# Kernel tuning notes

Measured on AMD Instinct MI355X. Metric: run time of the kernel, lower is better.

The kernel has to match this reference:

```python
import jax, jax.numpy as jnp
import numpy as np

N, E, C, NB, NE, G = 20000, 320000, 64, 8, 4, 16
L2 = 9          # (max_ell+1)^2 with max_ell=2
RMAX = 5.0
HID = 16        # nonlinear readout hidden width


def setup_inputs():
    key = jax.random.key(0)
    ks = jax.random.split(key, 16)
    positions = jax.random.uniform(ks[0], (N, 3), dtype=jnp.float32) * 3.0
    elems = jax.random.randint(ks[1], (N,), 0, NE)
    node_attrs = jax.nn.one_hot(elems, NE, dtype=jnp.float32)
    edge_index = jax.random.randint(ks[2], (2, E), 0, N)
    batch = jnp.sort(jax.random.randint(ks[3], (N,), 0, G))
    shifts = jnp.zeros((E, 3), jnp.float32)
    atomic_energies = jnp.array([-1.0, -2.0, -3.0, -4.0], jnp.float32)
    sc = lambda k, shp, fan: jax.random.normal(k, shp, jnp.float32) / np.sqrt(fan).astype(np.float32)
    W_embed = sc(ks[4], (NE, C), NE)
    W_up = sc(ks[5], (2, C, C), C)
    W1 = sc(ks[6], (2, NB, 64), NB)
    W2 = sc(ks[7], (2, 64, C), 64)
    W_out = sc(ks[8], (2, C, C), C)
    W_skip = sc(ks[9], (2, NE, C), NE)
    w_read0 = sc(ks[10], (C,), C)
    W_r1 = sc(ks[11], (C, HID), C)
    w_r2 = sc(ks[12], (HID,), HID)
    return dict(positions=positions, node_attrs=node_attrs, shifts=shifts,
                atomic_energies=atomic_energies, W_embed=W_embed, W_up=W_up,
                W1=W1, W2=W2, W_out=W_out, W_skip=W_skip, w_read0=w_read0,
                W_r1=W_r1, w_r2=w_r2, edge_index=edge_index, batch=batch)


def _sph_harm_l2(u):
    # component-normalized real spherical harmonics up to l=2 on unit vectors
    x, y, z = u[:, 0], u[:, 1], u[:, 2]
    s3, s5, s15 = jnp.sqrt(3.0), jnp.sqrt(5.0), jnp.sqrt(15.0)
    return jnp.stack([jnp.ones_like(x),
                      s3 * x, s3 * y, s3 * z,
                      s15 * x * y, s15 * y * z, 0.5 * s5 * (3.0 * z * z - 1.0),
                      s15 * x * z, 0.5 * s15 * (x * x - y * y)], axis=-1)


def _radial(r):
    # Bessel radial basis with polynomial cutoff (p=6)
    n = jnp.arange(1, NB + 1, dtype=jnp.float32)
    rb = jnp.sqrt(2.0 / RMAX) * jnp.sin(n * jnp.pi * r[:, None] / RMAX) / r[:, None]
    u = r / RMAX
    fc = 1.0 - 28.0 * u**6 + 48.0 * u**7 - 21.0 * u**8
    fc = jnp.where(u < 1.0, fc, 0.0)
    return rb * fc[:, None]


def _energy_contributions(positions, node_attrs, shifts, atomic_energies,
                          W_embed, W_up, W1, W2, W_out, W_skip,
                          w_read0, W_r1, w_r2, edge_index, batch):
    snd, rcv = edge_index[0], edge_index[1]
    vec = positions[snd] - positions[rcv] + shifts                  # [E,3]
    r = jnp.sqrt(jnp.sum(vec * vec, axis=-1) + 1e-12)               # [E]
    Y = _sph_harm_l2(vec / r[:, None])                              # [E,L2]
    ef = _radial(r)                                                 # [E,NB]
    # E0: per-element reference energies, summed per graph
    e0 = jax.ops.segment_sum(node_attrs @ atomic_energies, batch, num_segments=G)
    h0 = node_attrs @ W_embed                                       # [N,C] scalar feats
    h = jnp.zeros((positions.shape[0], L2, C), h0.dtype).at[:, 0, :].set(h0)
    readouts = [lambda s: s @ w_read0,
                lambda s: jax.nn.silu(s @ W_r1) @ w_r2]             # linear / nonlinear
    energies = [e0]
    for i in range(2):
        hu = jnp.einsum('nlc,cd->nld', h, W_up[i])                  # channel mix
        R = jax.nn.silu(ef @ W1[i]) @ W2[i]                         # radial MLP [E,C]
        s = jnp.einsum('elc,el->ec', hu[snd], Y)                    # equivariant contraction
        m = Y[:, :, None] * (R * s)[:, None, :]                     # [E,L2,C] messages
        agg = jax.ops.segment_sum(m, rcv, num_segments=positions.shape[0])
        h = jnp.einsum('nlc,cd->nld', agg, W_out[i])
        h = h.at[:, 0, :].add(node_attrs @ W_skip[i])               # scalar skip connection
        node_en = readouts[i](h[:, 0, :])                           # [N]
        energies.append(jax.ops.segment_sum(node_en, batch, num_segments=G))
    return jnp.stack(energies, axis=-1)                             # [G, num_interactions+1]


def reference(positions, node_attrs, shifts, atomic_energies, W_embed, W_up,
              W1, W2, W_out, W_skip, w_read0, W_r1, w_r2, edge_index, batch):
    contributions = _energy_contributions(positions, node_attrs, shifts,
        atomic_energies, W_embed, W_up, W1, W2, W_out, W_skip,
        w_read0, W_r1, w_r2, edge_index, batch)
    total_energy = jnp.sum(contributions, axis=-1)                  # [G]
    forces = -jax.grad(lambda p: jnp.sum(_energy_contributions(p, node_attrs,
        shifts, atomic_energies, W_embed, W_up, W1, W2, W_out, W_skip,
        w_read0, W_r1, w_r2, edge_index, batch)))(positions)        # [N,3]
    return total_energy, contributions, forces
```

## Files before the change

kernel.cpp:

```cpp
#include <hip/hip_runtime.h>
#include <cmath>

constexpr int N_  = 20000;
constexpr int E_  = 320000;
constexpr int NE_ = 4;
constexpr int G_  = 16;
constexpr int CAP = 96;
constexpr float RMAXF = 5.0f;
constexpr float PI_F  = 3.14159265358979323846f;
constexpr float S3  = 1.7320508075688772f;
constexpr float S5  = 2.2360679774997896f;
constexpr float S15 = 3.8729833462074170f;
constexpr float KC_ = 0.6324555320336759f;

typedef unsigned short u16;
typedef unsigned int   u32;
typedef _Float16 f16;
typedef _Float16 f16x2 __attribute__((ext_vector_type(2)));

#define DEV static __device__ __forceinline__

__device__ float g_fallback[110000000];

DEV float sigmoidf_(float x){ return 1.0f/(1.0f+__expf(-x)); }

DEV float b2f(u16 u){ return __uint_as_float(((u32)u)<<16); }
DEV u16  f2b(float f){
  u32 x = __float_as_uint(f);
  return (u16)((x + 0x7FFFu + ((x>>16)&1u)) >> 16);
}
DEV u16  f2h(float f){ union{f16 h; u16 u;} v; v.h=(f16)f; return v.u; }
DEV float h2f(u16 u){ union{u16 u2; f16 h;} v; v.u2=u; return (float)v.h; }

DEV f16x2 u2h(u32 x){ union{u32 u; f16x2 h;} v; v.u=x; return v.h; }
DEV u32 h2u(f16x2 h){ union{u32 u; f16x2 h;} v; v.h=h; return v.u; }
DEV u32 pkh(float a, float b){ f16x2 h; h.x=(f16)a; h.y=(f16)b; return h2u(h); }

DEV void st8(float* p, const float* d){
  ((float4*)p)[0] = make_float4(d[0],d[1],d[2],d[3]);
  ((float4*)p)[1] = make_float4(d[4],d[5],d[6],d[7]);
}
DEV void ld4(const float* __restrict__ p, float* d){
  float4 a = ((const float4*)p)[0];
  d[0]=a.x; d[1]=a.y; d[2]=a.z; d[3]=a.w;
}
DEV void ld4b(const u16* __restrict__ p, float* d){
  ushort4 a = *(const ushort4*)p;
  d[0]=b2f(a.x); d[1]=b2f(a.y); d[2]=b2f(a.z); d[3]=b2f(a.w);
}
DEV void ld4h(const u16* __restrict__ p, float* d){
  ushort4 a = *(const ushort4*)p;
  d[0]=h2f(a.x); d[1]=h2f(a.y); d[2]=h2f(a.z); d[3]=h2f(a.w);
}
DEV void st8b(u16* p, const float* d){
  uint4 v;
  v.x = (u32)f2b(d[0]) | ((u32)f2b(d[1])<<16);
  v.y = (u32)f2b(d[2]) | ((u32)f2b(d[3])<<16);
  v.z = (u32)f2b(d[4]) | ((u32)f2b(d[5])<<16);
  v.w = (u32)f2b(d[6]) | ((u32)f2b(d[7])<<16);
  *(uint4*)p = v;
}
DEV void st8h(u16* p, const float* d){
  uint4 v;
  v.x = pkh(d[0],d[1]); v.y = pkh(d[2],d[3]);
  v.z = pkh(d[4],d[5]); v.w = pkh(d[6],d[7]);
  *(uint4*)p = v;
}

__global__ void k_csr(const int* __restrict__ ei, int* __restrict__ cntR, int* __restrict__ cntS,
                      int* __restrict__ listR, int* __restrict__ listS){
  int e = blockIdx.x*256 + threadIdx.x;
  int s = ei[e], r = ei[E_+e];
  int p = atomicAdd(&cntR[r], 1); if (p < CAP) listR[r*CAP+p] = e;
  int q = atomicAdd(&cntS[s], 1); if (q < CAP) listS[s*CAP+q] = e;
}

__global__ void k_pre(const float* __restrict__ Wout0, const float* __restrict__ Wup1,
                      const float* __restrict__ Wskip0, const float* __restrict__ wread0,
                      float* __restrict__ WA, float* __restrict__ sa,
                      float* __restrict__ va, float* __restrict__ sv){
  int t = threadIdx.x;
  for (int idx=t; idx<4096; idx+=256){
    int c = idx>>6, d = idx&63;
    float acc=0.f;
    for (int m=0;m<64;++m) acc += Wout0[c*64+m]*Wup1[m*64+d];
    WA[idx]=acc;
  }
  {
    int k = t>>6, d = t&63;
    float acc=0.f;
    for (int m=0;m<64;++m) acc += Wskip0[k*64+m]*Wup1[m*64+d];
    sa[t]=acc;
  }
  if (t<64){
    float acc=0.f;
    for (int d=0;d<64;++d) acc += Wout0[t*64+d]*wread0[d];
    va[t]=acc;
  }
  if (t<4){
    float acc=0.f;
    for (int d=0;d<64;++d) acc += Wskip0[t*64+d]*wread0[d];
    sv[t]=acc;
  }
}

__global__ __launch_bounds__(256, 2)
void k_fwd_edge(const float* __restrict__ pos, const float* __restrict__ shifts,
                const int* __restrict__ ei,
                const float* __restrict__ W1g, const float* __restrict__ W2g,
                float* __restrict__ Y, float* __restrict__ u3,
                float* __restrict__ irr,
                u16* __restrict__ R0, u16* __restrict__ R1,
                u16* __restrict__ q0, u16* __restrict__ q1){
  __shared__ float sW1[1024];
  __shared__ u32   sW2h[4096];
  __shared__ u32   sAh[32*36];
  int t = threadIdx.x;
  for (int i=t;i<1024;i+=256) sW1[i]=W1g[i];
  for (int i=t;i<4096;i+=256){
    int L = i>>11, rem = i&2047, kp = rem>>6, c = rem&63;
    sW2h[i] = pkh(W2g[L*4096 + (2*kp)*64 + c], W2g[L*4096 + (2*kp+1)*64 + c]);
  }
  __syncthreads();
  int wid=t>>6, lane=t&63, q=lane>>3, j=lane&7, c0=j*8;
  int slot = wid*8 + q;
  int e = blockIdx.x*32 + slot;
  int snd = ei[e], rcv = ei[E_+e];
  float vx = pos[snd*3+0]-pos[rcv*3+0]+shifts[(size_t)e*3+0];
  float vy = pos[snd*3+1]-pos[rcv*3+1]+shifts[(size_t)e*3+1];
  float vz = pos[snd*3+2]-pos[rcv*3+2]+shifts[(size_t)e*3+2];
  float ss = vx*vx+vy*vy+vz*vz + 1e-12f;
  float rad = sqrtf(ss);
  float inv = 1.0f/rad;
  float x = vx*inv, y = vy*inv, z = vz*inv;
  float tt = rad*(1.0f/RMAXF);
  float fc = 0.0f, dfc = 0.0f;
  if (tt < 1.0f){
    float t2=tt*tt, t4=t2*t2, t5=t4*tt, t6=t5*tt, t7=t6*tt, t8=t7*tt;
    fc  = 1.0f - 28.0f*t6 + 48.0f*t7 - 21.0f*t8;
    dfc = (-168.0f*t5 + 336.0f*t6 - 168.0f*t7)*(1.0f/RMAXF);
  }
  float th = rad*(PI_F/RMAXF);
  float s1 = __sinf(th), c1 = __cosf(th);
  float base = KC_*inv*fc;
  float efv[8], gfv[8];
  {
    float sb = s1, cb = c1;
    #pragma unroll
    for (int b=0;b<8;++b){
      efv[b] = base*sb;
      float wb_ = (float)(b+1)*(PI_F/RMAXF);
      float rb  = KC_*sb*inv;
      float drb = KC_*(wb_*cb - sb*inv)*inv;
      gfv[b] = drb*fc + rb*dfc;
      float sn = sb*c1 + cb*s1;
      cb = cb*c1 - sb*s1;
      sb = sn;
    }
  }
  if (j==0){
    irr[e]=inv;
    u3[(size_t)e*3+0]=x; u3[(size_t)e*3+1]=y; u3[(size_t)e*3+2]=z;
    float* Ye = Y + (size_t)e*9;
    Ye[0]=1.0f;
    Ye[1]=S3*x; Ye[2]=S3*y; Ye[3]=S3*z;
    Ye[4]=S15*x*y; Ye[5]=S15*y*z;
    Ye[6]=0.5f*S5*(3.0f*z*z-1.0f);
    Ye[7]=S15*x*z;
    Ye[8]=0.5f*S15*(x*x-y*y);
  }
  u32* myAh = sAh + slot*36;
  for (int L=0; L<2; ++L){
    const float* w1 = sW1 + L*512;
    const u32*  w2h = sW2h + L*2048;
    float zz[8]={0,0,0,0,0,0,0,0};
    float wgv[8]={0,0,0,0,0,0,0,0};
    #pragma unroll 4
    for (int b=0;b<8;++b){
      float efb = efv[b], gfb = gfv[b];
      const float4* w=(const float4*)(w1 + b*64 + c0);
      float4 wa=w[0], wb=w[1];
      zz[0]+=efb*wa.x; zz[1]+=efb*wa.y; zz[2]+=efb*wa.z; zz[3]+=efb*wa.w;
      zz[4]+=efb*wb.x; zz[5]+=efb*wb.y; zz[6]+=efb*wb.z; zz[7]+=efb*wb.w;
      wgv[0]+=gfb*wa.x; wgv[1]+=gfb*wa.y; wgv[2]+=gfb*wa.z; wgv[3]+=gfb*wa.w;
      wgv[4]+=gfb*wb.x; wgv[5]+=gfb*wb.y; wgv[6]+=gfb*wb.z; wgv[7]+=gfb*wb.w;
    }
    float a[8], dv[8];
    #pragma unroll
    for (int i=0;i<8;++i){
      float sg = sigmoidf_(zz[i]);
      a[i]  = zz[i]*sg;
      float sp = sg*(1.0f + zz[i]*(1.0f - sg));
      dv[i] = wgv[i]*sp;
    }
    {
      uint4 av;
      av.x = pkh(a[0],a[1]); av.y = pkh(a[2],a[3]);
      av.z = pkh(a[4],a[5]); av.w = pkh(a[6],a[7]);
      *(uint4*)(myAh + 4*j) = av;
    }
    {
      float r0=0.f,r1=0.f,r2=0.f,r3=0.f,r4=0.f,r5=0.f,r6=0.f,r7=0.f;
      #pragma unroll 2
      for (int kp4=0; kp4<8; ++kp4){
        uint4 dq = *(const uint4*)(myAh + 4*kp4);
        #pragma unroll
        for (int i=0;i<4;++i){
          u32 du = (i==0)?dq.x:(i==1)?dq.y:(i==2)?dq.z:dq.w;
          f16x2 dh = u2h(du);
          const u32* wrow = w2h + (4*kp4+i)*64 + c0;
          uint4 w0 = *(const uint4*)(wrow);
          uint4 w1v = *(const uint4*)(wrow+4);
          r0 = __builtin_amdgcn_fdot2(dh, u2h(w0.x),  r0, false);
          r1 = __builtin_amdgcn_fdot2(dh, u2h(w0.y),  r1, false);
          r2 = __builtin_amdgcn_fdot2(dh, u2h(w0.z),  r2, false);
          r3 = __builtin_amdgcn_fdot2(dh, u2h(w0.w),  r3, false);
          r4 = __builtin_amdgcn_fdot2(dh, u2h(w1v.x), r4, false);
          r5 = __builtin_amdgcn_fdot2(dh, u2h(w1v.y), r5, false);
          r6 = __builtin_amdgcn_fdot2(dh, u2h(w1v.z), r6, false);
          r7 = __builtin_amdgcn_fdot2(dh, u2h(w1v.w), r7, false);
        }
      }
      float racc[8] = {r0,r1,r2,r3,r4,r5,r6,r7};
      st8b((L ? R1 : R0) + (size_t)e*64 + c0, racc);
    }
    {
      uint4 av;
      av.x = pkh(dv[0],dv[1]); av.y = pkh(dv[2],dv[3]);
      av.z = pkh(dv[4],dv[5]); av.w = pkh(dv[6],dv[7]);
      *(uint4*)(myAh + 4*j) = av;
    }
    {
      float r0=0.f,r1=0.f,r2=0.f,r3=0.f,r4=0.f,r5=0.f,r6=0.f,r7=0.f;
      #pragma unroll 2
      for (int kp4=0; kp4<8; ++kp4){
        uint4 dq = *(const uint4*)(myAh + 4*kp4);
        #pragma unroll
        for (int i=0;i<4;++i){
          u32 du = (i==0)?dq.x:(i==1)?dq.y:(i==2)?dq.z:dq.w;
          f16x2 dh = u2h(du);
          const u32* wrow = w2h + (4*kp4+i)*64 + c0;
          uint4 w0 = *(const uint4*)(wrow);
          uint4 w1v = *(const uint4*)(wrow+4);
          r0 = __builtin_amdgcn_fdot2(dh, u2h(w0.x),  r0, false);
          r1 = __builtin_amdgcn_fdot2(dh, u2h(w0.y),  r1, false);
          r2 = __builtin_amdgcn_fdot2(dh, u2h(w0.z),  r2, false);
          r3 = __builtin_amdgcn_fdot2(dh, u2h(w0.w),  r3, false);
          r4 = __builtin_amdgcn_fdot2(dh, u2h(w1v.x), r4, false);
          r5 = __builtin_amdgcn_fdot2(dh, u2h(w1v.y), r5, false);
          r6 = __builtin_amdgcn_fdot2(dh, u2h(w1v.z), r6, false);
          r7 = __builtin_amdgcn_fdot2(dh, u2h(w1v.w), r7, false);
        }
      }
      float qacc[8] = {r0,r1,r2,r3,r4,r5,r6,r7};
      st8h((L ? q1 : q0) + (size_t)e*64 + c0, qacc);
    }
  }
}

__global__ void k_e0(const float* __restrict__ attrs, const float* __restrict__ ae,
                     const int* __restrict__ batch, float* __restrict__ out){
  __shared__ float bins[G_];
  int t = threadIdx.x;
  if (t < G_) bins[t] = 0.f;
  __syncthreads();
  int n = blockIdx.x*256 + t;
  if (n < N_){
    float v = 0.f;
    #pragma unroll
    for (int k=0;k<NE_;++k) v += attrs[n*NE_+k]*ae[k];
    atomicAdd(&bins[batch[n]], v);
  }
  __syncthreads();
  if (t < G_){
    float b = bins[t];
    if (b != 0.f){
      atomicAdd(&out[t], b);
      atomicAdd(&out[G_ + t*3 + 0], b);
    }
  }
}

__global__ void k_wembup(const float* __restrict__ Wemb, const float* __restrict__ Wup0,
                         float* __restrict__ WembUp){
  int t = threadIdx.x; int k = t>>6, c = t&63;
  float acc = 0.f;
  for (int j=0;j<64;++j) acc += Wemb[k*64+j]*Wup0[j*64+c];
  WembUp[k*64+c] = acc;
}

__global__ void k_hu0(const float* __restrict__ attrs, const float* __restrict__ WembUp,
                      float* __restrict__ hu0){
  int i = blockIdx.x*256 + threadIdx.x;
  int n = i>>6, c = i&63;
  float acc = 0.f;
  #pragma unroll
  for (int k=0;k<NE_;++k) acc += attrs[n*NE_+k]*WembUp[k*64+c];
  hu0[i] = acc;
}

__global__ void k_agg0(const int* __restrict__ cntR, const int* __restrict__ listR,
                       const int* __restrict__ ei, const float* __restrict__ hu0,
                       const u16* __restrict__ R0, const float* __restrict__ Y,
                       float* __restrict__ agg0){
  int t = threadIdx.x; int n = blockIdx.x*4 + (t>>6); int c = t&63;
  float acc[9] = {0,0,0,0,0,0,0,0,0};
  int deg = min(cntR[n], CAP);
  #pragma unroll 2
  for (int j=0;j<deg;++j){
    int e = listR[n*CAP+j];
    int s = ei[e];
    float p = b2f(R0[(size_t)e*64+c])*hu0[(size_t)s*64+c];
    #pragma unroll
    for (int l=0;l<9;++l) acc[l] += Y[(size_t)e*9+l]*p;
  }
  #pragma unroll
  for (int l=0;l<9;++l) agg0[((size_t)n*9+l)*64+c] = acc[l];
}

__global__ void k_s1(const int* __restrict__ cntS, const int* __restrict__ listS,
                     const u16* __restrict__ hu1, const float* __restrict__ Y,
                     u16* __restrict__ s1){
  int t = threadIdx.x; int n = blockIdx.x*4 + (t>>6); int c = t&63;
  float hu[9];
  #pragma unroll
  for (int l=0;l<9;++l) hu[l] = b2f(hu1[((size_t)n*9+l)*64+c]);
  int deg = min(cntS[n], CAP);
  #pragma unroll 2
  for (int j=0;j<deg;++j){
    int e = listS[n*CAP+j];
    float acc = 0.f;
    #pragma unroll
    for (int l=0;l<9;++l) acc += hu[l]*Y[(size_t)e*9+l];
    s1[(size_t)e*64+c] = f2h(acc);
  }
}

__global__ void k_agg1(const int* __restrict__ cntR, const int* __restrict__ listR,
                       const u16* __restrict__ R1, const u16* __restrict__ s1,
                       float* __restrict__ agg1){
  int t = threadIdx.x; int n = blockIdx.x*4 + (t>>6); int c = t&63;
  float acc = 0.f;
  int deg = min(cntR[n], CAP);
  #pragma unroll 2
  for (int j=0;j<deg;++j){
    int e = listR[n*CAP+j];
    acc += b2f(R1[(size_t)e*64+c])*h2f(s1[(size_t)e*64+c]);
  }
  agg1[(size_t)n*64+c] = acc;
}

__global__ void k_dhu1(const int* __restrict__ cntS, const int* __restrict__ listS,
                       const int* __restrict__ ei, const u16* __restrict__ R1,
                       const float* __restrict__ ga1, const float* __restrict__ Y,
                       float* __restrict__ dhu1){
  int t = threadIdx.x; int n = blockIdx.x*4 + (t>>6); int c = t&63;
  float acc[9] = {0,0,0,0,0,0,0,0,0};
  int deg = min(cntS[n], CAP);
  #pragma unroll 2
  for (int j=0;j<deg;++j){
    int e = listS[n*CAP+j];
    int r = ei[E_+e];
    float ds = b2f(R1[(size_t)e*64+c])*ga1[(size_t)r*64+c];
    #pragma unroll
    for (int l=0;l<9;++l) acc[l] += Y[(size_t)e*9+l]*ds;
  }
  #pragma unroll
  for (int l=0;l<9;++l) dhu1[((size_t)n*9+l)*64+c] = acc[l];
}

template<bool TRANS, bool OUTB>
__global__ __launch_bounds__(256, 2)
void k_mm64(const float* __restrict__ in, const float* __restrict__ W,
            void* __restrict__ out, int rows, int lper,
            const float* __restrict__ attrs, const float* __restrict__ Wsk,
            const float* __restrict__ bias){
  __shared__ float sWT[64*68];
  __shared__ float sRow[4*68];
  int t = threadIdx.x;
  for (int i=t;i<4096;i+=256){
    int k=i&63, c=i>>6;
    sWT[c*68+k] = TRANS ? W[c*64+k] : W[k*64+c];
  }
  __syncthreads();
  int wid = t>>6, c = t&63;
  float wcol[64];
  {
    const float4* wp = (const float4*)(sWT + c*68);
    #pragma unroll
    for (int kk=0;kk<16;++kk){
      float4 w4 = wp[kk];
      wcol[4*kk+0]=w4.x; wcol[4*kk+1]=w4.y; wcol[4*kk+2]=w4.z; wcol[4*kk+3]=w4.w;
    }
  }
  float* myRow = sRow + wid*68;
  for (int it=0; it<8; ++it){
    int row = (blockIdx.x*8+it)*4 + wid;
    myRow[c] = in[(size_t)row*64+c];
    float acc = 0.f;
    #pragma unroll
    for (int kk=0;kk<16;++kk){
      float4 r4 = ((const float4*)myRow)[kk];
      acc += r4.x*wcol[4*kk+0] + r4.y*wcol[4*kk+1] + r4.z*wcol[4*kk+2] + r4.w*wcol[4*kk+3];
    }
    if (lper==1 || (row % 9)==0){
      int n = (lper==1) ? row : (row/9);
      if (attrs){
        #pragma unroll
        for (int k=0;k<NE_;++k) acc += attrs[n*NE_+k]*Wsk[k*64+c];
      }
      if (bias) acc += bias[c];
    }
    if (OUTB) ((u16*)out)[(size_t)row*64+c] = f2b(acc);
    else      ((float*)out)[(size_t)row*64+c] = acc;
  }
}

__global__ void k_read0(const float* __restrict__ agg0, const float* __restrict__ va,
                        const float* __restrict__ sv, const float* __restrict__ attrs,
                        const int* __restrict__ batch, float* __restrict__ out){
  __shared__ float bins[G_];
  int t = threadIdx.x;
  if (t < G_) bins[t] = 0.f;
  __syncthreads();
  int lane = t & 63, wid = t >> 6;
  int grp = lane >> 3, j = lane & 7;
  int n = blockIdx.x*32 + wid*8 + grp;
  const float* hp = agg0 + (size_t)n*576 + j*8;
  const float* wp = va + j*8;
  float4 h0 = ((const float4*)hp)[0], h4 = ((const float4*)hp)[1];
  float4 w0v = ((const float4*)wp)[0], w4v = ((const float4*)wp)[1];
  float v = h0.x*w0v.x + h0.y*w0v.y + h0.z*w0v.z + h0.w*w0v.w
          + h4.x*w4v.x + h4.y*w4v.y + h4.z*w4v.z + h4.w*w4v.w;
  v += __shfl_xor(v,1,64); v += __shfl_xor(v,2,64); v += __shfl_xor(v,4,64);
  if (j==0){
    v += attrs[n*NE_+0]*sv[0] + attrs[n*NE_+1]*sv[1]
       + attrs[n*NE_+2]*sv[2] + attrs[n*NE_+3]*sv[3];
    atomicAdd(&bins[batch[n]], v);
  }
  __syncthreads();
  if (t < G_){
    float b = bins[t];
    if (b != 0.f){
      atomicAdd(&out[t], b);
      atomicAdd(&out[G_ + t*3 + 1], b);
    }
  }
}

__global__ void k_read1(const float* __restrict__ h2, const float* __restrict__ Wr1,
                        const float* __restrict__ wr2, const int* __restrict__ batch,
                        float* __restrict__ spz, float* __restrict__ out){
  __shared__ float sW[64*16];
  __shared__ float sA[256];
  __shared__ float bins[G_];
  int t = threadIdx.x;
  for (int i=t;i<1024;i+=256) sW[i]=Wr1[i];
  if (t < G_) bins[t] = 0.f;
  __syncthreads();
  int n = blockIdx.x*16 + (t>>4); int j = t&15;
  float z = 0.f;
  #pragma unroll 16
  for (int c=0;c<64;++c) z += h2[(size_t)n*64+c]*sW[c*16+j];
  float sg = sigmoidf_(z);
  float a  = z*sg;
  float sp = sg*(1.0f + z*(1.0f - sg));
  float w2v = wr2[j];
  spz[n*16+j] = sp*w2v;
  sA[t] = a*w2v;
  __syncthreads();
  if (j==0){
    float s = 0.f;
    #pragma unroll
    for (int k=0;k<16;++k) s += sA[t+k];
    atomicAdd(&bins[batch[n]], s);
  }
  __syncthreads();
  if (t < G_){
    float b = bins[t];
    if (b != 0.f){
      atomicAdd(&out[t], b);
      atomicAdd(&out[G_ + t*3 + 2], b);
    }
  }
}

__global__ void k_dh2(const float* __restrict__ Wr1, const float* __restrict__ spz,
                      float* __restrict__ dh2){
  int i = blockIdx.x*256 + threadIdx.x;
  int n = i>>6, c = i&63;
  float acc = 0.f;
  #pragma unroll
  for (int j=0;j<16;++j) acc += Wr1[c*16+j]*spz[n*16+j];
  dh2[i] = acc;
}

__global__ __launch_bounds__(256, 4)
void k_bedge_all(const int* __restrict__ ei, const float* __restrict__ Y,
             const float* __restrict__ u3, const float* __restrict__ irr,
             const u16* __restrict__ R0b, const u16* __restrict__ R1b,
             const float* __restrict__ ga1, const u16* __restrict__ ga0,
             const float* __restrict__ hu0, const u16* __restrict__ hu1,
             const u16* __restrict__ q0b, const u16* __restrict__ q1b,
             float* __restrict__ gF){
  int t = threadIdx.x;
  int wid=t>>6, lane=t&63, q=lane>>4, j=lane&15, c0=j*4;
  int slot = wid*4+q;
  int e = blockIdx.x*16 + slot;
  int snd = ei[e], rcv = ei[E_+e];
  float Yl[9];
  #pragma unroll
  for (int l=0;l<9;++l) Yl[l] = Y[(size_t)e*9+l];
  ushort4 huv1[9];
  #pragma unroll
  for (int l=0;l<9;++l) huv1[l] = *(const ushort4*)(hu1 + ((size_t)snd*9 + l)*64 + c0);
  ushort4 gv0[9];
  #pragma unroll
  for (int l=0;l<9;++l) gv0[l] = *(const ushort4*)(ga0 + ((size_t)rcv*9 + l)*64 + c0);
  float T1[4];  ld4(ga1 + (size_t)rcv*64 + c0, T1);
  float hu0v[4]; ld4(hu0 + (size_t)snd*64 + c0, hu0v);
  float R1v[4]; ld4b(R1b + (size_t)e*64 + c0, R1v);
  float R0v[4]; ld4b(R0b + (size_t)e*64 + c0, R0v);
  float q1v[4]; ld4h(q1b + (size_t)e*64 + c0, q1v);
  float q0v[4]; ld4h(q0b + (size_t)e*64 + c0, q0v);
  float dyp[9];
  float dR1[4];
  {
    float ds1[4], sA[4];
    #pragma unroll
    for (int i=0;i<4;++i){ ds1[i]=R1v[i]*T1[i]; sA[i]=0.f; }
    #pragma unroll
    for (int l=0;l<9;++l){
      float h0v=b2f(huv1[l].x), h1v=b2f(huv1[l].y), h2v=b2f(huv1[l].z), h3v=b2f(huv1[l].w);
      float Ylv = Yl[l];
      sA[0]+=h0v*Ylv; sA[1]+=h1v*Ylv; sA[2]+=h2v*Ylv; sA[3]+=h3v*Ylv;
      dyp[l] = ds1[0]*h0v + ds1[1]*h1v + ds1[2]*h2v + ds1[3]*h3v;
    }
    #pragma unroll
    for (int i=0;i<4;++i) dR1[i]=sA[i]*T1[i];
  }
  float dR0[4];
  {
    float P[4], T0[4];
    #pragma unroll
    for (int i=0;i<4;++i){ P[i]=R0v[i]*hu0v[i]; T0[i]=0.f; }
    #pragma unroll
    for (int l=0;l<9;++l){
      float g0=b2f(gv0[l].x), g1=b2f(gv0[l].y), g2=b2f(gv0[l].z), g3=b2f(gv0[l].w);
      float Ylv = Yl[l];
      T0[0]+=g0*Ylv; T0[1]+=g1*Ylv; T0[2]+=g2*Ylv; T0[3]+=g3*Ylv;
      dyp[l] += g0*P[0] + g1*P[1] + g2*P[2] + g3*P[3];
    }
    #pragma unroll
    for (int i=0;i<4;++i) dR0[i]=hu0v[i]*T0[i];
  }
  float dy[9];
  #pragma unroll
  for (int l=1;l<9;++l){
    float v=dyp[l];
    v += __shfl_xor(v,1,64); v += __shfl_xor(v,2,64);
    v += __shfl_xor(v,4,64); v += __shfl_xor(v,8,64);
    dy[l]=v;
  }
  float dr = q1v[0]*dR1[0]+q1v[1]*dR1[1]+q1v[2]*dR1[2]+q1v[3]*dR1[3]
           + q0v[0]*dR0[0]+q0v[1]*dR0[1]+q0v[2]*dR0[2]+q0v[3]*dR0[3];
  dr += __shfl_xor(dr,1,64); dr += __shfl_xor(dr,2,64);
  dr += __shfl_xor(dr,4,64); dr += __shfl_xor(dr,8,64);
  float x = u3[(size_t)e*3+0], y = u3[(size_t)e*3+1], zz = u3[(size_t)e*3+2];
  float invr = irr[e];
  float dux = S3*dy[1] + S15*(y*dy[4] + zz*dy[7] + x*dy[8]);
  float duy = S3*dy[2] + S15*(x*dy[4] + zz*dy[5] - y*dy[8]);
  float duz = S3*dy[3] + S15*(y*dy[5] + x*dy[7]) + 3.0f*S5*zz*dy[6];
  float udot = x*dux + y*duy + zz*duz;
  float gx = dr*x + invr*(dux - x*udot);
  float gy = dr*y + invr*(duy - y*udot);
  float gz = dr*zz + invr*(duz - zz*udot);
  if (j==0){
    float* gp2 = gF + (size_t)e*3;
    gp2[0]=gx; gp2[1]=gy; gp2[2]=gz;
  }
}

__global__ void k_fsum(const int* __restrict__ cnts, const int* __restrict__ lists,
                       const float* __restrict__ gF, float* __restrict__ F){
  int t = threadIdx.x;
  int lane = t & 63, wid = t >> 6;
  int sub = lane >> 3, j = lane & 7;
  int n = blockIdx.x*32 + wid*8 + sub;
  const int* cntR = cnts;       const int* cntS = cnts + N_;
  const int* listR = lists;     const int* listS = lists + (size_t)N_*CAP;
  float fx=0.f, fy=0.f, fz=0.f;
  int dRn = min(cntR[n], CAP);
  for (int k=j;k<dRn;k+=8){
    int e = listR[n*CAP+k];
    fx += gF[(size_t)e*3+0]; fy += gF[(size_t)e*3+1]; fz += gF[(size_t)e*3+2];
  }
  int dSn = min(cntS[n], CAP);
  for (int k=j;k<dSn;k+=8){
    int e = listS[n*CAP+k];
    fx -= gF[(size_t)e*3+0]; fy -= gF[(size_t)e*3+1]; fz -= gF[(size_t)e*3+2];
  }
  fx += __shfl_xor(fx,1,64); fy += __shfl_xor(fy,1,64); fz += __shfl_xor(fz,1,64);
  fx += __shfl_xor(fx,2,64); fy += __shfl_xor(fy,2,64); fz += __shfl_xor(fz,2,64);
  fx += __shfl_xor(fx,4,64); fy += __shfl_xor(fy,4,64); fz += __shfl_xor(fz,4,64);
  if (j==0){
    F[n*3+0]=fx; F[n*3+1]=fy; F[n*3+2]=fz;
  }
}

extern "C" void kernel_launch(void* const* d_in, const int* in_sizes, int n_in,
                              void* d_out, int out_size, void* d_ws, size_t ws_size,
                              hipStream_t stream){
  (void)in_sizes; (void)n_in;
  const float* pos    = (const float*)d_in[0];
  const float* attrs  = (const float*)d_in[1];
  const float* shifts = (const float*)d_in[2];
  const float* ae     = (const float*)d_in[3];
  const float* Wemb   = (const float*)d_in[4];
  const float* Wup    = (const float*)d_in[5];
  const float* W1     = (const float*)d_in[6];
  const float* W2     = (const float*)d_in[7];
  const float* Wout   = (const float*)d_in[8];
  const float* Wskip  = (const float*)d_in[9];
  const float* wread0 = (const float*)d_in[10];
  const float* Wr1    = (const float*)d_in[11];
  const float* wr2    = (const float*)d_in[12];
  const int*   ei     = (const int*)d_in[13];
  const int*   batch  = (const int*)d_in[14];
  float* out = (float*)d_out;

  const size_t NEED = 430000000;
  char* base;
  if (ws_size >= NEED){
    base = (char*)d_ws;
  } else {
    void* p = nullptr;
    hipGetSymbolAddress(&p, HIP_SYMBOL(g_fallback));
    base = (char*)p;
  }
  size_t off = 0;
  auto alloc = [&](size_t bytes)->char*{
    char* p = base + off;
    off += ((bytes + 255)/256)*256;
    return p;
  };
  float* Y    = (float*)alloc((size_t)E_*9*4);
  float* u3   = (float*)alloc((size_t)E_*3*4);
  float* irr  = (float*)alloc((size_t)E_*4);
  u16*   R0   = (u16*)  alloc((size_t)E_*64*2);
  u16*   R1   = (u16*)  alloc((size_t)E_*64*2);
  u16*   q0   = (u16*)  alloc((size_t)E_*64*2);
  u16*   q1   = (u16*)  alloc((size_t)E_*64*2);
  u16*   s1b  = (u16*)  alloc((size_t)E_*64*2);
  float* gF   = (float*)alloc((size_t)E_*3*4);
  float* hu0  = (float*)alloc((size_t)N_*64*4);
  u16*   hu1  = (u16*)  alloc((size_t)N_*9*64*2);
  float* agg0 = (float*)alloc((size_t)N_*9*64*4);
  float* agg1 = (float*)alloc((size_t)N_*64*4);
  float* h2   = (float*)alloc((size_t)N_*64*4);
  float* spz  = (float*)alloc((size_t)N_*16*4);
  float* dh2  = (float*)alloc((size_t)N_*64*4);
  float* ga1  = (float*)alloc((size_t)N_*64*4);
  u16*   ga0  = (u16*)  alloc((size_t)N_*9*64*2);
  float* WembUp = (float*)alloc(256*4);
  float* WA   = (float*)alloc(4096*4);
  float* sa   = (float*)alloc(256*4);
  float* va   = (float*)alloc(64*4);
  float* sv   = (float*)alloc(4*4);
  int* cnts  = (int*)alloc((size_t)2*N_*4);
  int* lists = (int*)alloc((size_t)2*N_*CAP*4);
  int* cntR = cnts;          int* cntS = cnts + N_;
  int* listR = lists;        int* listS = lists + (size_t)N_*CAP;
  float* dhu1 = agg0;
  float* F = out + G_ + G_*3;

  hipMemsetAsync(d_out, 0, (size_t)out_size*sizeof(float), stream);
  hipMemsetAsync(cnts, 0, (size_t)2*N_*sizeof(int), stream);

  k_csr     <<<E_/256, 256, 0, stream>>>(ei, cntR, cntS, listR, listS);
  k_fwd_edge<<<E_/32, 256, 0, stream>>>(pos, shifts, ei, W1, W2, Y, u3, irr, R0, R1, q0, q1);
  k_wembup  <<<1, 256, 0, stream>>>(Wemb, Wup, WembUp);
  k_pre     <<<1, 256, 0, stream>>>(Wout, Wup + 4096, Wskip, wread0, WA, sa, va, sv);
  k_e0      <<<(N_+255)/256, 256, 0, stream>>>(attrs, ae, batch, out);
  k_hu0     <<<N_*64/256, 256, 0, stream>>>(attrs, WembUp, hu0);
  k_agg0    <<<N_/4, 256, 0, stream>>>(cntR, listR, ei, hu0, R0, Y, agg0);
  k_mm64<false,true><<<N_*9/32, 256, 0, stream>>>(agg0, WA, hu1, N_*9, 9, attrs, sa, nullptr);
  k_read0   <<<N_/32, 256, 0, stream>>>(agg0, va, sv, attrs, batch, out);
  k_s1      <<<N_/4, 256, 0, stream>>>(cntS, listS, hu1, Y, s1b);
  k_agg1    <<<N_/4, 256, 0, stream>>>(cntR, listR, R1, s1b, agg1);
  k_mm64<false,false><<<N_/32, 256, 0, stream>>>(agg1, Wout + 4096, h2, N_, 1, attrs, Wskip + 256, nullptr);
  k_read1   <<<N_/16, 256, 0, stream>>>(h2, Wr1, wr2, batch, spz, out);

  k_dh2     <<<N_*64/256, 256, 0, stream>>>(Wr1, spz, dh2);
  k_mm64<true,false><<<N_/32, 256, 0, stream>>>(dh2, Wout + 4096, ga1, N_, 1, nullptr, nullptr, nullptr);
  k_dhu1    <<<N_/4, 256, 0, stream>>>(cntS, listS, ei, R1, ga1, Y, dhu1);
  k_mm64<true,true><<<N_*9/32, 256, 0, stream>>>(dhu1, WA, ga0, N_*9, 9, nullptr, nullptr, va);
  k_bedge_all<<<E_/16, 256, 0, stream>>>(ei, Y, u3, irr, R0, R1, ga1, ga0, hu0, hu1, q0, q1, gF);
  k_fsum    <<<N_/32, 256, 0, stream>>>(cnts, lists, gF, F);
}
```

Baseline: 886.6 us.

## Replace per-edge radial MLP with interpolated precomputed radial table

```diff
diff --git a/kernel.cpp b/kernel.cpp
--- a/kernel.cpp
+++ b/kernel.cpp
@@ -6,6 +6,7 @@
 constexpr int NE_ = 4;
 constexpr int G_  = 16;
 constexpr int CAP = 96;
+constexpr int TAB = 4096;
 constexpr float RMAXF = 5.0f;
 constexpr float PI_F  = 3.14159265358979323846f;
 constexpr float S3  = 1.7320508075688772f;
@@ -36,10 +37,6 @@
 DEV u32 h2u(f16x2 h){ union{u32 u; f16x2 h;} v; v.h=h; return v.u; }
 DEV u32 pkh(float a, float b){ f16x2 h; h.x=(f16)a; h.y=(f16)b; return h2u(h); }
 
-DEV void st8(float* p, const float* d){
-  ((float4*)p)[0] = make_float4(d[0],d[1],d[2],d[3]);
-  ((float4*)p)[1] = make_float4(d[4],d[5],d[6],d[7]);
-}
 DEV void ld4(const float* __restrict__ p, float* d){
   float4 a = ((const float4*)p)[0];
   d[0]=a.x; d[1]=a.y; d[2]=a.z; d[3]=a.w;
@@ -105,13 +102,8 @@
 }
 
 __global__ __launch_bounds__(256, 2)
-void k_fwd_edge(const float* __restrict__ pos, const float* __restrict__ shifts,
-                const int* __restrict__ ei,
-                const float* __restrict__ W1g, const float* __restrict__ W2g,
-                float* __restrict__ Y, float* __restrict__ u3,
-                float* __restrict__ irr,
-                u16* __restrict__ R0, u16* __restrict__ R1,
-                u16* __restrict__ q0, u16* __restrict__ q1){
+void k_rtab(const float* __restrict__ W1g, const float* __restrict__ W2g,
+            u16* __restrict__ tab){
   __shared__ float sW1[1024];
   __shared__ u32   sW2h[4096];
   __shared__ u32   sAh[32*36];
@@ -124,15 +116,10 @@
   __syncthreads();
   int wid=t>>6, lane=t&63, q=lane>>3, j=lane&7, c0=j*8;
   int slot = wid*8 + q;
-  int e = blockIdx.x*32 + slot;
-  int snd = ei[e], rcv = ei[E_+e];
-  float vx = pos[snd*3+0]-pos[rcv*3+0]+shifts[(size_t)e*3+0];
-  float vy = pos[snd*3+1]-pos[rcv*3+1]+shifts[(size_t)e*3+1];
-  float vz = pos[snd*3+2]-pos[rcv*3+2]+shifts[(size_t)e*3+2];
-  float ss = vx*vx+vy*vy+vz*vz + 1e-12f;
-  float rad = sqrtf(ss);
+  int knot = blockIdx.x*32 + slot;
+  bool valid = (knot <= TAB);
+  float rad = fmaxf((float)knot * (RMAXF/(float)TAB), 1e-6f);
   float inv = 1.0f/rad;
-  float x = vx*inv, y = vy*inv, z = vz*inv;
   float tt = rad*(1.0f/RMAXF);
   float fc = 0.0f, dfc = 0.0f;
   if (tt < 1.0f){
@@ -157,17 +144,6 @@
       cb = cb*c1 - sb*s1;
       sb = sn;
     }
-  }
-  if (j==0){
-    irr[e]=inv;
-    u3[(size_t)e*3+0]=x; u3[(size_t)e*3+1]=y; u3[(size_t)e*3+2]=z;
-    float* Ye = Y + (size_t)e*9;
-    Ye[0]=1.0f;
-    Ye[1]=S3*x; Ye[2]=S3*y; Ye[3]=S3*z;
-    Ye[4]=S15*x*y; Ye[5]=S15*y*z;
-    Ye[6]=0.5f*S5*(3.0f*z*z-1.0f);
-    Ye[7]=S15*x*z;
-    Ye[8]=0.5f*S15*(x*x-y*y);
   }
   u32* myAh = sAh + slot*36;
   for (int L=0; L<2; ++L){
@@ -222,7 +198,7 @@
         }
       }
       float racc[8] = {r0,r1,r2,r3,r4,r5,r6,r7};
-      st8b((L ? R1 : R0) + (size_t)e*64 + c0, racc);
+      if (valid) st8h(tab + (size_t)knot*256 + L*64 + c0, racc);
     }
     {
       uint4 av;
@@ -253,9 +229,68 @@
         }
       }
       float qacc[8] = {r0,r1,r2,r3,r4,r5,r6,r7};
-      st8h((L ? q1 : q0) + (size_t)e*64 + c0, qacc);
-    }
-  }
+      if (valid) st8h(tab + (size_t)knot*256 + 128 + L*64 + c0, qacc);
+    }
+  }
+}
+
+__global__ void k_fwd_edge(const float* __restrict__ pos, const float* __restrict__ shifts,
+                const int* __restrict__ ei, const u16* __restrict__ tab,
+                float* __restrict__ Y, float* __restrict__ u3,
+                float* __restrict__ irr,
+                u16* __restrict__ R0, u16* __restrict__ R1,
+                u16* __restrict__ q0, u16* __restrict__ q1){
+  int t = threadIdx.x;
+  int wid=t>>6, lane=t&63, q=lane>>3, j=lane&7, c0=j*8;
+  int slot = wid*8 + q;
+  int e = blockIdx.x*32 + slot;
+  int snd = ei[e], rcv = ei[E_+e];
+  float vx = pos[snd*3+0]-pos[rcv*3+0]+shifts[(size_t)e*3+0];
+  float vy = pos[snd*3+1]-pos[rcv*3+1]+shifts[(size_t)e*3+1];
+  float vz = pos[snd*3+2]-pos[rcv*3+2]+shifts[(size_t)e*3+2];
+  float ss = vx*vx+vy*vy+vz*vz + 1e-12f;
+  float rad = sqrtf(ss);
+  float inv = 1.0f/rad;
+  float x = vx*inv, y = vy*inv, z = vz*inv;
+  if (j==0){
+    irr[e]=inv;
+    u3[(size_t)e*3+0]=x; u3[(size_t)e*3+1]=y; u3[(size_t)e*3+2]=z;
+    float* Ye = Y + (size_t)e*9;
+    Ye[0]=1.0f;
+    Ye[1]=S3*x; Ye[2]=S3*y; Ye[3]=S3*z;
+    Ye[4]=S15*x*y; Ye[5]=S15*y*z;
+    Ye[6]=0.5f*S5*(3.0f*z*z-1.0f);
+    Ye[7]=S15*x*z;
+    Ye[8]=0.5f*S15*(x*x-y*y);
+  }
+  float vR0[8], vR1[8], vq0[8], vq1[8];
+  if (rad < RMAXF){
+    float xi = rad * ((float)TAB/RMAXF);
+    int i0 = (int)xi; if (i0 > TAB-1) i0 = TAB-1;
+    float f = xi - (float)i0;
+    float g = 1.0f - f;
+    const u16* ra = tab + (size_t)i0*256 + c0;
+    const u16* rb = ra + 256;
+    #pragma unroll
+    for (int sec=0; sec<4; ++sec){
+      ushort4 a0 = *(const ushort4*)(ra + sec*64);
+      ushort4 a1 = *(const ushort4*)(ra + sec*64 + 4);
+      ushort4 b0 = *(const ushort4*)(rb + sec*64);
+      ushort4 b1 = *(const ushort4*)(rb + sec*64 + 4);
+      float* dst = (sec==0)?vR0:(sec==1)?vR1:(sec==2)?vq0:vq1;
+      dst[0]=h2f(a0.x)*g+h2f(b0.x)*f; dst[1]=h2f(a0.y)*g+h2f(b0.y)*f;
+      dst[2]=h2f(a0.z)*g+h2f(b0.z)*f; dst[3]=h2f(a0.w)*g+h2f(b0.w)*f;
+      dst[4]=h2f(a1.x)*g+h2f(b1.x)*f; dst[5]=h2f(a1.y)*g+h2f(b1.y)*f;
+      dst[6]=h2f(a1.z)*g+h2f(b1.z)*f; dst[7]=h2f(a1.w)*g+h2f(b1.w)*f;
+    }
+  } else {
+    #pragma unroll
+    for (int i=0;i<8;++i){ vR0[i]=0.f; vR1[i]=0.f; vq0[i]=0.f; vq1[i]=0.f; }
+  }
+  st8b(R0 + (size_t)e*64 + c0, vR0);
+  st8b(R1 + (size_t)e*64 + c0, vR1);
+  st8h(q0 + (size_t)e*64 + c0, vq0);
+  st8h(q1 + (size_t)e*64 + c0, vq1);
 }
 
 __global__ void k_e0(const float* __restrict__ attrs, const float* __restrict__ ae,
@@ -653,6 +688,7 @@
   u16*   q1   = (u16*)  alloc((size_t)E_*64*2);
   u16*   s1b  = (u16*)  alloc((size_t)E_*64*2);
   float* gF   = (float*)alloc((size_t)E_*3*4);
+  u16*   tab  = (u16*)  alloc((size_t)(TAB+1)*256*2);
   float* hu0  = (float*)alloc((size_t)N_*64*4);
   u16*   hu1  = (u16*)  alloc((size_t)N_*9*64*2);
   float* agg0 = (float*)alloc((size_t)N_*9*64*4);
@@ -678,7 +714,8 @@
   hipMemsetAsync(cnts, 0, (size_t)2*N_*sizeof(int), stream);
 
   k_csr     <<<E_/256, 256, 0, stream>>>(ei, cntR, cntS, listR, listS);
-  k_fwd_edge<<<E_/32, 256, 0, stream>>>(pos, shifts, ei, W1, W2, Y, u3, irr, R0, R1, q0, q1);
+  k_rtab    <<<(TAB+1+31)/32, 256, 0, stream>>>(W1, W2, tab);
+  k_fwd_edge<<<E_/32, 256, 0, stream>>>(pos, shifts, ei, tab, Y, u3, irr, R0, R1, q0, q1);
   k_wembup  <<<1, 256, 0, stream>>>(Wemb, Wup, WembUp);
   k_pre     <<<1, 256, 0, stream>>>(Wout, Wup + 4096, Wskip, wread0, WA, sa, va, sv);
   k_e0      <<<(N_+255)/256, 256, 0, stream>>>(attrs, ae, batch, out);
```

New measurement: 792.7 us. 1.12x faster.
